# Kernel tuning notes

Hardware: AMD Instinct MI355X
Metric: run time of the kernel (lower is better)

The kernel has to match this reference:

```python
import jax, jax.numpy as jnp
import numpy as np

N_NODES = 100000
N_EDGES = 1600000
N_PAIRS = 500000
IN_C, HID_C, OUT_C = 128, 128, 128


def setup_inputs() -> dict:
    key = jax.random.key(0)
    ks = jax.random.split(key, 12)
    def lin(k, fan_in, shape):
        b = 1.0 / np.sqrt(fan_in)
        return jax.random.uniform(k, shape, jnp.float32, -b, b)
    return {
        "x": jax.random.normal(ks[0], (N_NODES, IN_C), jnp.float32),
        "edge_index": jax.random.randint(ks[1], (2, N_EDGES), 0, N_NODES),
        "edge_pairs": jax.random.randint(ks[2], (2, N_PAIRS), 0, N_NODES),
        "W1": lin(ks[3], IN_C, (IN_C, HID_C)),
        "b1": jnp.zeros((HID_C,), jnp.float32),
        "W2": lin(ks[4], HID_C, (HID_C, OUT_C)),
        "b2": jnp.zeros((OUT_C,), jnp.float32),
        "Wm1": lin(ks[5], 2 * OUT_C, (2 * OUT_C, HID_C)),
        "bm1": lin(ks[6], 2 * OUT_C, (HID_C,)),
        "Wm2": lin(ks[7], HID_C, (HID_C, 1)),
        "bm2": lin(ks[8], HID_C, (1,)),
    }


def reference(x, edge_index, edge_pairs, W1, b1, W2, b2, Wm1, bm1, Wm2, bm2):
    N = x.shape[0]
    loop = jnp.arange(N, dtype=edge_index.dtype)
    row = jnp.concatenate([edge_index[0], loop])  # source nodes (+self loops)
    col = jnp.concatenate([edge_index[1], loop])  # target nodes (+self loops)
    # symmetric GCN normalization: deg^{-1/2}[row] * deg^{-1/2}[col]
    deg = jax.ops.segment_sum(jnp.ones(col.shape, x.dtype), col, num_segments=N)
    dinv = jnp.where(deg > 0, jax.lax.rsqrt(deg), 0.0)
    norm = dinv[row] * dinv[col]  # [E+N]

    def gcn_conv(h, W, b):
        h = h @ W  # transform first (PyG GCNConv lin has no bias)
        msg = h[row] * norm[:, None]
        return jax.ops.segment_sum(msg, col, num_segments=N) + b

    h = jax.nn.relu(gcn_conv(x, W1, b1))
    h = gcn_conv(h, W2, b2)  # dropout p=0.0 -> identity

    src, dst = edge_pairs[0], edge_pairs[1]
    ef = jnp.concatenate([h[src], h[dst]], axis=-1)  # [P, 2*out]
    out = jax.nn.relu(ef @ Wm1 + bm1) @ Wm2 + bm2
    return out.squeeze(-1)
```

## Files before the change

kernel.cpp:

```cpp
#include <hip/hip_runtime.h>
#include <hip/hip_fp16.h>

#define NCH 128
#define G_NODES 256
#define EPB 4096
#define RCAP 4864
#define MAXNB 512
#define KST 40

typedef __attribute__((ext_vector_type(8))) short short8;
typedef _Float16 half8 __attribute__((ext_vector_type(8)));
typedef __attribute__((ext_vector_type(4))) float floatx4;

static inline size_t align256(size_t x){ return (x + 255) & ~(size_t)255; }

__global__ __launch_bounds__(256) void binA_kernel(
    const int* __restrict__ row, const int* __restrict__ col,
    int* __restrict__ gcur, unsigned* __restrict__ bucketed, int E, int NB,
    const float* __restrict__ W1, const float* __restrict__ W2,
    const float* __restrict__ Wm1, const float* __restrict__ b2,
    const float* __restrict__ bm1, short* __restrict__ planes,
    float* __restrict__ bm1p, float* __restrict__ zbias){
  __shared__ int cnt[MAXNB];
  __shared__ int lbase[MAXNB];
  __shared__ int gbase[MAXNB];
  __shared__ unsigned sorted[EPB];
  __shared__ unsigned short binOf[EPB];
  __shared__ int sh[256];
  __shared__ int carry;
  __shared__ float w2row[128];
  int t = threadIdx.x;
  int e0 = blockIdx.x * EPB;
  int ecnt = min(EPB, E - e0);
  for (int i = t; i < NB; i += 256) cnt[i] = 0;
  if (t == 0) carry = 0;
  __syncthreads();
  unsigned rec[16]; int bn[16]; int rk[16];
  #pragma unroll
  for (int i = 0; i < 16; i++){
    int e = e0 + i * 256 + t;
    if (e < E){
      int r = row[e], c = col[e];
      bn[i]  = c >> 8;
      rec[i] = (unsigned)r | ((unsigned)(c & 255) << 17);
      rk[i]  = atomicAdd(&cnt[bn[i]], 1);
    } else bn[i] = -1;
  }
  __syncthreads();
  for (int start = 0; start < NB; start += 256){
    int i = start + t;
    int v = (i < NB) ? cnt[i] : 0;
    sh[t] = v; __syncthreads();
    for (int off = 1; off < 256; off <<= 1){
      int val = (t >= off) ? sh[t - off] : 0;
      __syncthreads(); sh[t] += val; __syncthreads();
    }
    if (i < NB) lbase[i] = sh[t] - v + carry;
    __syncthreads();
    if (t == 255) carry += sh[255];
    __syncthreads();
  }
  for (int i = t; i < NB; i += 256){
    int c = cnt[i];
    gbase[i] = (c > 0) ? atomicAdd(&gcur[i], c) : 0;
  }
  __syncthreads();
  #pragma unroll
  for (int i = 0; i < 16; i++){
    if (bn[i] >= 0){
      int pos = lbase[bn[i]] + rk[i];
      sorted[pos] = rec[i];
      binOf[pos]  = (unsigned short)bn[i];
    }
  }
  __syncthreads();
  for (int idx = t; idx < ecnt; idx += 256){
    int b = binOf[idx];
    int gpos = gbase[b] + (idx - lbase[b]);
    if (gpos < RCAP) bucketed[(size_t)b * RCAP + gpos] = sorted[idx];
  }
  {
    int gid = blockIdx.x * 256 + t;
    if (gid < 16384){
      int k = gid >> 7, n = gid & 127;
      float x = W1[gid];
      unsigned u = __float_as_uint(x);
      short hs = (short)(u >> 16);
      float hf = __uint_as_float(u & 0xFFFF0000u);
      short ls = (short)(__float_as_uint(x - hf) >> 16);
      planes[n * 128 + k]         = hs;
      planes[16384 + n * 128 + k] = ls;
    }
  }
  if (blockIdx.x >= 64 && blockIdx.x < 192){
    int b = blockIdx.x - 64;
    if (t < 128) w2row[t] = W2[b * 128 + t];
    __syncthreads();
    int mat = t >> 7, n = t & 127;
    const float* Wsrc = Wm1 + (size_t)mat * 16384;
    float acc = 0.f;
    #pragma unroll 4
    for (int j = 0; j < 128; j++) acc = fmaf(w2row[j], Wsrc[j * 128 + n], acc);
    __half hh = __float2half(acc);
    __half ll = __float2half(acc - __half2float(hh));
    planes[(size_t)(4 + 2 * mat) * 16384 + n * 128 + b] = __half_as_short(hh);
    planes[(size_t)(5 + 2 * mat) * 16384 + n * 128 + b] = __half_as_short(ll);
  } else if (blockIdx.x == 192){
    if (t < 128){
      float acc = bm1[t];
      for (int j = 0; j < 128; j++)
        acc += b2[j] * (Wm1[j * 128 + t] + Wm1[(128 + j) * 128 + t]);
      bm1p[t] = acc;
      zbias[t] = 0.f;
    }
  }
}

__global__ __launch_bounds__(512, 4) void fused_gemm_binB(
    const float* __restrict__ X, const short* __restrict__ Whi_,
    const short* __restrict__ Wlo_, __half* __restrict__ O, int nrows, int gemmBlocks,
    const unsigned* __restrict__ bucketed, const int* __restrict__ gcur,
    int* __restrict__ rows_sorted, int* __restrict__ offs,
    int* __restrict__ counts, float* __restrict__ dinv, int N){
  __shared__ __align__(16) char smem[40960];
  int t = threadIdx.x;
  if (blockIdx.x < gemmBlocks){
    short* Xhi = (short*)smem;
    short* Xlo = Xhi + 128 * KST;
    short* Whi = Xlo + 128 * KST;
    short* Wlo = Whi + 128 * KST;
    int w = t >> 6, lane = t & 63;
    int m = lane & 15, q = lane >> 4;
    int row0 = blockIdx.x * 128;
    floatx4 acc[8];
    #pragma unroll
    for (int ct = 0; ct < 8; ct++) acc[ct] = (floatx4)0.f;
    for (int kc = 0; kc < 4; kc++){
      int k0 = kc * 32;
      __syncthreads();
      #pragma unroll
      for (int qq = 0; qq < 2; qq++){
        int f = t + 512 * qq;
        int r = f >> 3, kq = f & 7;
        int gr = row0 + r;
        int grc = (gr < nrows) ? gr : 0;
        float4 v = *(const float4*)(X + (size_t)grc * NCH + k0 + kq * 4);
        short h[4], l[4];
        float vv[4] = {v.x, v.y, v.z, v.w};
        #pragma unroll
        for (int j = 0; j < 4; j++){
          unsigned u = __float_as_uint(vv[j]);
          h[j] = (short)(u >> 16);
          float hf = __uint_as_float(u & 0xFFFF0000u);
          l[j] = (short)(__float_as_uint(vv[j] - hf) >> 16);
        }
        *(uint2*)(Xhi + r * KST + kq * 4) = *(uint2*)h;
        *(uint2*)(Xlo + r * KST + kq * 4) = *(uint2*)l;
      }
      {
        int n = t >> 2, kq = t & 3;
        *(uint4*)(Whi + n * KST + kq * 8) = *(const uint4*)(Whi_ + n * NCH + k0 + kq * 8);
        *(uint4*)(Wlo + n * KST + kq * 8) = *(const uint4*)(Wlo_ + n * NCH + k0 + kq * 8);
      }
      __syncthreads();
      short8 a_hi = *(const short8*)(Xhi + (w * 16 + m) * KST + q * 8);
      short8 a_lo = *(const short8*)(Xlo + (w * 16 + m) * KST + q * 8);
      #pragma unroll
      for (int ct = 0; ct < 8; ct++){
        short8 b_hi = *(const short8*)(Whi + (ct * 16 + m) * KST + q * 8);
        short8 b_lo = *(const short8*)(Wlo + (ct * 16 + m) * KST + q * 8);
        acc[ct] = __builtin_amdgcn_mfma_f32_16x16x32_bf16(a_hi, b_hi, acc[ct], 0, 0, 0);
        acc[ct] = __builtin_amdgcn_mfma_f32_16x16x32_bf16(a_lo, b_hi, acc[ct], 0, 0, 0);
        acc[ct] = __builtin_amdgcn_mfma_f32_16x16x32_bf16(a_hi, b_lo, acc[ct], 0, 0, 0);
      }
    }
    #pragma unroll
    for (int r = 0; r < 4; r++){
      int grow = row0 + w * 16 + q * 4 + r;
      if (grow < nrows){
        #pragma unroll
        for (int ct = 0; ct < 8; ct++)
          O[(size_t)grow * NCH + ct * 16 + m] = __float2half(acc[ct][r]);
      }
    }
  } else {
    int b = blockIdx.x - gemmBlocks;
    unsigned* ledge = (unsigned*)smem;
    int* cnt  = (int*)(smem + RCAP * 4);
    int* cnt2 = cnt + 256;
    int* lex  = cnt2 + 256;
    int* sh   = lex + 256;
    int size = min(gcur[b], RCAP);
    int n0 = b * G_NODES;
    if (t < 256){ cnt[t] = 0; cnt2[t] = 0; }
    __syncthreads();
    for (int i = t; i < size; i += 512){
      unsigned v = bucketed[(size_t)b * RCAP + i];
      ledge[i] = v;
      atomicAdd(&cnt[v >> 17], 1);
    }
    __syncthreads();
    {
      int v = (t < 256) ? cnt[t] : 0;
      if (t < 256) sh[t] = v;
      __syncthreads();
      for (int off = 1; off < 256; off <<= 1){
        int val = (t >= off && t < 256) ? sh[t - off] : 0;
        __syncthreads();
        if (t < 256) sh[t] += val;
        __syncthreads();
      }
      if (t < 256){
        lex[t] = sh[t] - v;
        int n = n0 + t;
        if (n < N){
          counts[n] = v;
          offs[n]   = b * RCAP + sh[t] - v;
          dinv[n]   = rsqrtf((float)v + 1.0f);
        }
      }
    }
    __syncthreads();
    for (int i = t; i < size; i += 512){
      unsigned v = ledge[i];
      int node = v >> 17;
      int pos = lex[node] + atomicAdd(&cnt2[node], 1);
      rows_sorted[(size_t)b * RCAP + pos] = (int)(v & 0x1FFFFu);
    }
  }
}

template<int NCT>
__global__ __launch_bounds__(512, 4) void gemm_f16k(
    const __half* __restrict__ X,
    const short* __restrict__ Whi0, const short* __restrict__ Wlo0,
    const short* __restrict__ Whi1, const short* __restrict__ Wlo1,
    const float* __restrict__ scale, int do_scale,
    __half* __restrict__ O0, __half* __restrict__ O1, int nrows){
  __shared__ short Xs[128 * KST];
  __shared__ short Whs[NCT * 16 * KST];
  __shared__ short Wls[NCT * 16 * KST];
  int t = threadIdx.x;
  int w = t >> 6, lane = t & 63;
  int m = lane & 15, q = lane >> 4;
  int row0 = blockIdx.x * 128;
  floatx4 acc[NCT];
  #pragma unroll
  for (int ct = 0; ct < NCT; ct++) acc[ct] = (floatx4)0.f;

  for (int kc = 0; kc < 4; kc++){
    int k0 = kc * 32;
    __syncthreads();
    {
      int r = t >> 2, kq = t & 3;
      int gr = row0 + r;
      int grc = (gr < nrows) ? gr : 0;
      *(uint4*)(Xs + r * KST + kq * 8) = *(const uint4*)(X + (size_t)grc * NCH + k0 + kq * 8);
    }
    #pragma unroll
    for (int i = t; i < NCT * 16 * 4; i += 512){
      int n = i >> 2, kq = i & 3;
      const short* sh = (n < 128) ? (Whi0 + n * NCH) : (Whi1 + (n - 128) * NCH);
      const short* sl = (n < 128) ? (Wlo0 + n * NCH) : (Wlo1 + (n - 128) * NCH);
      *(uint4*)(Whs + n * KST + kq * 8) = *(const uint4*)(sh + k0 + kq * 8);
      *(uint4*)(Wls + n * KST + kq * 8) = *(const uint4*)(sl + k0 + kq * 8);
    }
    __syncthreads();
    half8 a = *(const half8*)(Xs + (w * 16 + m) * KST + q * 8);
    #pragma unroll
    for (int ct = 0; ct < NCT; ct++){
      half8 bh = *(const half8*)(Whs + (ct * 16 + m) * KST + q * 8);
      half8 bl = *(const half8*)(Wls + (ct * 16 + m) * KST + q * 8);
      acc[ct] = __builtin_amdgcn_mfma_f32_16x16x32_f16(a, bh, acc[ct], 0, 0, 0);
      acc[ct] = __builtin_amdgcn_mfma_f32_16x16x32_f16(a, bl, acc[ct], 0, 0, 0);
    }
  }
  #pragma unroll
  for (int r = 0; r < 4; r++){
    int grow = row0 + w * 16 + q * 4 + r;
    if (grow < nrows){
      float sc = do_scale ? scale[grow] : 1.0f;
      #pragma unroll
      for (int ct = 0; ct < NCT; ct++){
        __half val = __float2half(acc[ct][r] * sc);
        if (ct < 8) O0[(size_t)grow * NCH + ct * 16 + m] = val;
        else        O1[(size_t)grow * NCH + (ct - 8) * 16 + m] = val;
      }
    }
  }
}

__global__ __launch_bounds__(256) void agg_kernel(
    const __half* __restrict__ s, const float* __restrict__ dinv,
    const int* __restrict__ offs, const int* __restrict__ counts,
    const int* __restrict__ rows_sorted, const float* __restrict__ bias,
    __half* __restrict__ outp, int N, int do_relu, int edge_dinv){
  int wave = (int)((blockIdx.x * blockDim.x + threadIdx.x) >> 6);
  int lane = threadIdx.x & 63;
  if (wave >= N) return;
  int c = wave;
  int g = lane >> 4, h = lane & 15;
  float di = dinv[c];
  float wself = edge_dinv ? di : 1.0f;
  float acc[8] = {0.f,0.f,0.f,0.f,0.f,0.f,0.f,0.f};
  if (g == 0){
    uint4 v = *(const uint4*)(s + (size_t)c * NCH + h * 8);
    const __half2* hp = (const __half2*)&v;
    #pragma unroll
    for (int i = 0; i < 4; i++){
      float2 f = __half22float2(hp[i]);
      acc[2*i] = fmaf(wself, f.x, acc[2*i]); acc[2*i+1] = fmaf(wself, f.y, acc[2*i+1]);
    }
  }
  int off = offs[c], cnt = counts[c];
  for (int chunk = 0; chunk < cnt; chunk += 64){
    int nn = min(64, cnt - chunk);
    int myidx = (lane < nn) ? rows_sorted[off + chunk + lane] : 0;
    float mydinv = 1.0f;
    if (edge_dinv && lane < nn) mydinv = dinv[myidx];
    int jmax = (nn + 3) >> 2;
    #pragma unroll 8
    for (int j = 0; j < jmax; j++){
      int e = 4 * j + g;
      int r  = __shfl(myidx, e & 63, 64);
      float dr = edge_dinv ? __shfl(mydinv, e & 63, 64) : 1.0f;
      if (e < nn){
        uint4 v = *(const uint4*)(s + (size_t)r * NCH + h * 8);
        const __half2* hp = (const __half2*)&v;
        #pragma unroll
        for (int i = 0; i < 4; i++){
          float2 f = __half22float2(hp[i]);
          acc[2*i] = fmaf(dr, f.x, acc[2*i]); acc[2*i+1] = fmaf(dr, f.y, acc[2*i+1]);
        }
      }
    }
  }
  #pragma unroll
  for (int i = 0; i < 8; i++){
    acc[i] += __shfl_xor(acc[i], 16, 64);
    acc[i] += __shfl_xor(acc[i], 32, 64);
  }
  if (g == 0){
    float4 b0 = *(const float4*)(bias + h * 8);
    float4 b1 = *(const float4*)(bias + h * 8 + 4);
    float o[8];
    o[0] = di*acc[0]+b0.x; o[1] = di*acc[1]+b0.y; o[2] = di*acc[2]+b0.z; o[3] = di*acc[3]+b0.w;
    o[4] = di*acc[4]+b1.x; o[5] = di*acc[5]+b1.y; o[6] = di*acc[6]+b1.z; o[7] = di*acc[7]+b1.w;
    if (do_relu){
      #pragma unroll
      for (int i = 0; i < 8; i++) o[i] = fmaxf(o[i], 0.f);
    }
    __half2 packed[4];
    #pragma unroll
    for (int i = 0; i < 4; i++) packed[i] = __floats2half2_rn(o[2*i], o[2*i+1]);
    *(uint4*)(outp + (size_t)c * NCH + h * 8) = *(uint4*)packed;
  }
}

__global__ __launch_bounds__(256) void pair_kernel(
    const __half* __restrict__ A, const __half* __restrict__ B,
    const int* __restrict__ src, const int* __restrict__ dst,
    const float* __restrict__ bm1, const float* __restrict__ Wm2,
    const float* __restrict__ bm2, float* __restrict__ outp, int P){
  int gwave = (int)((blockIdx.x * blockDim.x + threadIdx.x) >> 6);
  int lane  = threadIdx.x & 63;
  int nw    = (int)((gridDim.x * blockDim.x) >> 6);
  int g = lane >> 4, h = lane & 15;
  float bb[8], ww[8];
  {
    float4 t0 = *(const float4*)(bm1 + h * 8);
    float4 t1 = *(const float4*)(bm1 + h * 8 + 4);
    bb[0]=t0.x; bb[1]=t0.y; bb[2]=t0.z; bb[3]=t0.w;
    bb[4]=t1.x; bb[5]=t1.y; bb[6]=t1.z; bb[7]=t1.w;
    float4 w0 = *(const float4*)(Wm2 + h * 8);
    float4 w1 = *(const float4*)(Wm2 + h * 8 + 4);
    ww[0]=w0.x; ww[1]=w0.y; ww[2]=w0.z; ww[3]=w0.w;
    ww[4]=w1.x; ww[5]=w1.y; ww[6]=w1.z; ww[7]=w1.w;
  }
  float bsc = bm2[0];
  const __half* basep = (g & 1) ? B : A;
  const int* idxp = (g & 1) ? dst : src;
  int s = g >> 1;
  for (int p0 = gwave * 16; p0 < P; p0 += nw * 16){
    int pi[8]; uint4 v[8];
    #pragma unroll
    for (int k = 0; k < 8; k++){
      int p = p0 + 2 * k + s;
      pi[k] = p;
      int px = (p < P) ? p : P - 1;
      int node = idxp[px];
      v[k] = *(const uint4*)(basep + (size_t)node * NCH + h * 8);
    }
    float pr[8];
    #pragma unroll
    for (int k = 0; k < 8; k++){
      const __half2* hp = (const __half2*)&v[k];
      float f[8];
      #pragma unroll
      for (int i = 0; i < 4; i++){
        float2 t2 = __half22float2(hp[i]);
        f[2*i] = t2.x; f[2*i+1] = t2.y;
      }
      float p_ = 0.f;
      #pragma unroll
      for (int i = 0; i < 8; i++){
        float o = __shfl_xor(f[i], 16, 64);
        p_ += fmaxf(f[i] + o + bb[i], 0.f) * ww[i];
      }
      pr[k] = p_;
    }
    #pragma unroll
    for (int k = 0; k < 8; k++){
      #pragma unroll
      for (int d = 1; d <= 8; d <<= 1) pr[k] += __shfl_xor(pr[k], d, 64);
    }
    if ((lane & 31) == 0){
      #pragma unroll
      for (int k = 0; k < 8; k++)
        if (pi[k] < P) outp[pi[k]] = pr[k] + bsc;
    }
  }
}


extern "C" void kernel_launch(void* const* d_in, const int* in_sizes, int n_in,
                              void* d_out, int out_size, void* d_ws, size_t ws_size,
                              hipStream_t stream){
  const float* x   = (const float*)d_in[0];
  const int*   ei  = (const int*)  d_in[1];
  const int*   ep  = (const int*)  d_in[2];
  const float* W1  = (const float*)d_in[3];
  const float* b1  = (const float*)d_in[4];
  const float* W2  = (const float*)d_in[5];
  const float* b2  = (const float*)d_in[6];
  const float* Wm1 = (const float*)d_in[7];
  const float* bm1 = (const float*)d_in[8];
  const float* Wm2 = (const float*)d_in[9];
  const float* bm2 = (const float*)d_in[10];
  float* outp = (float*)d_out;

  const int N = in_sizes[0] / NCH;
  const int E = in_sizes[1] / 2;
  const int P = in_sizes[2] / 2;
  const int NB = (N + G_NODES - 1) / G_NODES;

  char* base = (char*)d_ws;
  size_t off = 0;
  int*      counts      = (int*)     (base + off); off = align256(off + (size_t)N * 4);
  int*      offs        = (int*)     (base + off); off = align256(off + (size_t)N * 4);
  float*    dinv        = (float*)   (base + off); off = align256(off + (size_t)N * 4);
  int*      gcur        = (int*)     (base + off); off = align256(off + (size_t)NB * 4);
  unsigned* bucketed    = (unsigned*)(base + off); off = align256(off + (size_t)NB * RCAP * 4);
  int*      rows_sorted = (int*)     (base + off); off = align256(off + (size_t)NB * RCAP * 4);
  short*    planes      = (short*)   (base + off); off = align256(off + (size_t)8 * 16384 * 2);
  float*    bm1p        = (float*)   (base + off); off = align256(off + (size_t)256 * 4);
  float*    zbias       = (float*)   (base + off); off = align256(off + (size_t)128 * 4);
  __half*   s1buf       = (__half*)  (base + off); off = align256(off + (size_t)N * NCH * 2);
  __half*   h1buf       = (__half*)  (base + off); off = align256(off + (size_t)N * NCH * 2);
  __half*   zbuf        = (__half*)  (base + off); off = align256(off + (size_t)N * NCH * 2);
  __half*   sA          = (__half*)  (base + off); off = align256(off + (size_t)N * NCH * 2);
  __half*   sB          = (__half*)  (base + off); off = align256(off + (size_t)N * NCH * 2);
  (void)ws_size; (void)n_in; (void)out_size;

  short* W1hi = planes + 0 * 16384;
  short* W1lo = planes + 1 * 16384;
  short* Wahi = planes + 4 * 16384;
  short* Walo = planes + 5 * 16384;
  short* Wbhi = planes + 6 * 16384;
  short* Wblo = planes + 7 * 16384;

  const int* row = ei;
  const int* col = ei + E;
  const int* psrc = ep;
  const int* pdst = ep + P;

  int gemm_grid = (N + 127) / 128;
  int agg_grid  = (N + 3) / 4;
  int binA_grid = (E + EPB - 1) / EPB;
  if (binA_grid < 193) binA_grid = 193;

  hipMemsetAsync(gcur, 0, (size_t)NB * 4, stream);
  binA_kernel<<<binA_grid, 256, 0, stream>>>(row, col, gcur, bucketed, E, NB,
                                             W1, W2, Wm1, b2, bm1, planes, bm1p, zbias);
  fused_gemm_binB<<<gemm_grid + NB, 512, 0, stream>>>(
      x, W1hi, W1lo, s1buf, N, gemm_grid,
      bucketed, gcur, rows_sorted, offs, counts, dinv, N);
  agg_kernel<<<agg_grid, 256, 0, stream>>>(s1buf, dinv, offs, counts, rows_sorted, b1, h1buf, N, 1, 1);
  agg_kernel<<<agg_grid, 256, 0, stream>>>(h1buf, dinv, offs, counts, rows_sorted, zbias, zbuf, N, 0, 1);
  gemm_f16k<16><<<gemm_grid, 512, 0, stream>>>(zbuf, Wahi, Walo, Wbhi, Wblo, dinv, 0, sA, sB, N);
  pair_kernel<<<8192, 256, 0, stream>>>(sA, sB, psrc, pdst, bm1p, Wm2, bm2, outp, P);
}
```

Baseline: 371.5 us.

## Bin link-prediction pairs by source-node bucket to localize gathers

A new pbin_kernel groups query pairs into 256-node buckets keyed by source node. Each pair is packed with its src, dst and original index into a 64-bit record and stored in a fixed-capacity slab per bucket. The pair kernel then runs two blocks per bucket, broadcasting records with shuffles, so gathers from the source-side table hit a small node range and should cache better. The cost is an extra binning pass, scattered output writes, and a coarser grid. Any bucket that overflows PCAP silently drops pairs, so correctness depends on the pairs being spread roughly evenly.

```diff
diff --git a/kernel.cpp b/kernel.cpp
--- a/kernel.cpp
+++ b/kernel.cpp
@@ -7,6 +7,8 @@
 #define RCAP 4864
 #define MAXNB 512
 #define KST 40
+#define PEPB 4096
+#define PCAP 1600
 
 typedef __attribute__((ext_vector_type(8))) short short8;
 typedef _Float16 half8 __attribute__((ext_vector_type(8)));
@@ -116,6 +118,43 @@
   }
 }
 
+__global__ __launch_bounds__(256) void pbin_kernel(
+    const int* __restrict__ src, const int* __restrict__ dst,
+    int* __restrict__ pcur, unsigned long long* __restrict__ pslab, int P, int NB){
+  __shared__ int cnt[MAXNB];
+  __shared__ int gbase[MAXNB];
+  int t = threadIdx.x;
+  int p0 = blockIdx.x * PEPB;
+  for (int i = t; i < NB; i += 256) cnt[i] = 0;
+  __syncthreads();
+  unsigned long long rec[16]; int bn[16]; int rk[16];
+  #pragma unroll
+  for (int i = 0; i < 16; i++){
+    int p = p0 + i * 256 + t;
+    if (p < P){
+      int s = src[p], d = dst[p];
+      bn[i] = s >> 8;
+      rec[i] = (unsigned long long)p
+             | ((unsigned long long)d << 19)
+             | ((unsigned long long)s << 36);
+      rk[i] = atomicAdd(&cnt[bn[i]], 1);
+    } else bn[i] = -1;
+  }
+  __syncthreads();
+  for (int i = t; i < NB; i += 256){
+    int c = cnt[i];
+    gbase[i] = (c > 0) ? atomicAdd(&pcur[i], c) : 0;
+  }
+  __syncthreads();
+  #pragma unroll
+  for (int i = 0; i < 16; i++){
+    if (bn[i] >= 0){
+      int pos = gbase[bn[i]] + rk[i];
+      if (pos < PCAP) pslab[(size_t)bn[i] * PCAP + pos] = rec[i];
+    }
+  }
+}
+
 __global__ __launch_bounds__(512, 4) void fused_gemm_binB(
     const float* __restrict__ X, const short* __restrict__ Whi_,
     const short* __restrict__ Wlo_, __half* __restrict__ O, int nrows, int gemmBlocks,
@@ -357,14 +396,16 @@
   }
 }
 
-__global__ __launch_bounds__(256) void pair_kernel(
+__global__ __launch_bounds__(256) void pair2_kernel(
     const __half* __restrict__ A, const __half* __restrict__ B,
-    const int* __restrict__ src, const int* __restrict__ dst,
+    const int* __restrict__ pcur, const unsigned long long* __restrict__ pslab,
     const float* __restrict__ bm1, const float* __restrict__ Wm2,
-    const float* __restrict__ bm2, float* __restrict__ outp, int P){
-  int gwave = (int)((blockIdx.x * blockDim.x + threadIdx.x) >> 6);
-  int lane  = threadIdx.x & 63;
-  int nw    = (int)((gridDim.x * blockDim.x) >> 6);
+    const float* __restrict__ bm2, float* __restrict__ outp, int P, int NB){
+  int bucket = blockIdx.x >> 1;
+  int half = blockIdx.x & 1;
+  if (bucket >= NB) return;
+  int t = threadIdx.x;
+  int wv = t >> 6, lane = t & 63;
   int g = lane >> 4, h = lane & 15;
   float bb[8], ww[8];
   {
@@ -379,16 +420,27 @@
   }
   float bsc = bm2[0];
   const __half* basep = (g & 1) ? B : A;
-  const int* idxp = (g & 1) ? dst : src;
   int s = g >> 1;
-  for (int p0 = gwave * 16; p0 < P; p0 += nw * 16){
+  int cnt = min(pcur[bucket], PCAP);
+  const unsigned long long* slab = pslab + (size_t)bucket * PCAP;
+  int nch = (cnt + 63) >> 6;
+  for (int ch = half; ch < nch; ch += 2){
+    int base = ch * 64 + wv * 16;
+    unsigned long long rec = 0;
+    {
+      int pl = base + (lane & 15);
+      if (pl < cnt) rec = slab[pl];
+    }
     int pi[8]; uint4 v[8];
     #pragma unroll
     for (int k = 0; k < 8; k++){
-      int p = p0 + 2 * k + s;
-      pi[k] = p;
-      int px = (p < P) ? p : P - 1;
-      int node = idxp[px];
+      int j = 2 * k + s;
+      unsigned long long r = __shfl(rec, j, 64);
+      int orig = (int)(r & 0x7FFFFULL);
+      int dnode = (int)((r >> 19) & 0x1FFFFULL);
+      int snode = (int)((r >> 36) & 0x1FFFFULL);
+      int node = (g & 1) ? dnode : snode;
+      pi[k] = (base + j < cnt) ? orig : -1;
       v[k] = *(const uint4*)(basep + (size_t)node * NCH + h * 8);
     }
     float pr[8];
@@ -417,7 +469,7 @@
     if ((lane & 31) == 0){
       #pragma unroll
       for (int k = 0; k < 8; k++)
-        if (pi[k] < P) outp[pi[k]] = pr[k] + bsc;
+        if (pi[k] >= 0) outp[pi[k]] = pr[k] + bsc;
     }
   }
 }
@@ -449,9 +501,11 @@
   int*      counts      = (int*)     (base + off); off = align256(off + (size_t)N * 4);
   int*      offs        = (int*)     (base + off); off = align256(off + (size_t)N * 4);
   float*    dinv        = (float*)   (base + off); off = align256(off + (size_t)N * 4);
-  int*      gcur        = (int*)     (base + off); off = align256(off + (size_t)NB * 4);
+  int*      gcur        = (int*)     (base + off); off = align256(off + (size_t)2 * NB * 4);
   unsigned* bucketed    = (unsigned*)(base + off); off = align256(off + (size_t)NB * RCAP * 4);
   int*      rows_sorted = (int*)     (base + off); off = align256(off + (size_t)NB * RCAP * 4);
+  unsigned long long* pslab = (unsigned long long*)(base + off);
+                                                   off = align256(off + (size_t)NB * PCAP * 8);
   short*    planes      = (short*)   (base + off); off = align256(off + (size_t)8 * 16384 * 2);
   float*    bm1p        = (float*)   (base + off); off = align256(off + (size_t)256 * 4);
   float*    zbias       = (float*)   (base + off); off = align256(off + (size_t)128 * 4);
@@ -462,6 +516,8 @@
   __half*   sB          = (__half*)  (base + off); off = align256(off + (size_t)N * NCH * 2);
   (void)ws_size; (void)n_in; (void)out_size;
 
+  int* pcur = gcur + NB;
+
   short* W1hi = planes + 0 * 16384;
   short* W1lo = planes + 1 * 16384;
   short* Wahi = planes + 4 * 16384;
@@ -479,7 +535,8 @@
   int binA_grid = (E + EPB - 1) / EPB;
   if (binA_grid < 193) binA_grid = 193;
 
-  hipMemsetAsync(gcur, 0, (size_t)NB * 4, stream);
+  hipMemsetAsync(gcur, 0, (size_t)2 * NB * 4, stream);
+  pbin_kernel<<<(P + PEPB - 1) / PEPB, 256, 0, stream>>>(psrc, pdst, pcur, pslab, P, NB);
   binA_kernel<<<binA_grid, 256, 0, stream>>>(row, col, gcur, bucketed, E, NB,
                                              W1, W2, Wm1, b2, bm1, planes, bm1p, zbias);
   fused_gemm_binB<<<gemm_grid + NB, 512, 0, stream>>>(
@@ -488,5 +545,5 @@
   agg_kernel<<<agg_grid, 256, 0, stream>>>(s1buf, dinv, offs, counts, rows_sorted, b1, h1buf, N, 1, 1);
   agg_kernel<<<agg_grid, 256, 0, stream>>>(h1buf, dinv, offs, counts, rows_sorted, zbias, zbuf, N, 0, 1);
   gemm_f16k<16><<<gemm_grid, 512, 0, stream>>>(zbuf, Wahi, Walo, Wbhi, Wblo, dinv, 0, sA, sB, N);
-  pair_kernel<<<8192, 256, 0, stream>>>(sA, sB, psrc, pdst, bm1p, Wm2, bm2, outp, P);
-}
+  pair2_kernel<<<2 * NB, 256, 0, stream>>>(sA, sB, pcur, pslab, bm1p, Wm2, bm2, outp, P, NB);
+}
```

Result: slower. 410.7 us (+10.6%).
